# Kernel tuning notes

Hardware: AMD Instinct MI355X
Metric: run time of the kernel (lower is better)

The kernel has to match this reference:

```python
import jax, jax.numpy as jnp
import numpy as np

E, T, D, K = 8, 32768, 1024, 2  # experts, tokens, model dim, topk


def setup_inputs() -> dict:
    key = jax.random.key(0)
    k1, k2, k3, k4 = jax.random.split(key, 4)
    return {
        "tokens": jax.random.normal(k1, (T, D), jnp.float32),
        "router_w": jax.random.normal(k2, (E, D), jnp.float32) * 0.02,
        "w1": jax.random.normal(k3, (E, D, D), jnp.float32) * 0.02,
        "w2": jax.random.normal(k4, (E, D, D), jnp.float32) * 0.02,
    }


def reference(tokens, router_w, w1, w2):
    # Router: softmax over experts, then top-k (order of k irrelevant: combine is a sum)
    scores = jax.nn.softmax(tokens @ router_w.T, axis=-1)          # [T, E]
    topv, topi = jax.lax.top_k(scores, K)                          # [T, K]
    n_tok = tokens.shape[0]
    # Per-token gate weight for each expert (sum of topk weights where index==e).
    gate = jnp.zeros((n_tok, E), tokens.dtype).at[
        jnp.arange(n_tok)[:, None], topi
    ].add(topv)                                                    # [T, E]
    # Dense per-expert MLP, masked/weighted combine == sorted gather + scatter-sum
    out = jnp.zeros_like(tokens)
    for e in range(E):  # fixed small expert count; not a data-dim loop
        h = jax.nn.gelu(tokens @ w1[e], approximate=False)         # [T, D]
        out = out + gate[:, e:e + 1] * (h @ w2[e])                 # [T, D]
    return out
```

## Files before the change

kernel.cpp:

```cpp
#include <hip/hip_runtime.h>
#include <hip/hip_bf16.h>
#include <math.h>
#include <stdint.h>

#define TOK 32768
#define DIM 1024
#define NE 8
#define NSEG 16
#define BMCAP (2 * TOK + NSEG * 256)

#define C_CNT(s) ((s) * 16)
#define C_CUR(s) (256 + (s) * 16)
#define C_SEG(s) (512 + (s))

typedef __attribute__((ext_vector_type(8))) short bf16x8;
typedef __attribute__((ext_vector_type(4))) float f32x4;
typedef unsigned short ushort_t;

__device__ __forceinline__ unsigned short f2b(float x) {
  union { float f; unsigned u; } v; v.f = x;
  unsigned r = v.u + 0x7fffu + ((v.u >> 16) & 1u);
  return (unsigned short)(r >> 16);
}

__device__ __forceinline__ float gelu_fast(float x) {
  const float y2 = -1.5957691216057308f * x * fmaf(0.044715f, x * x, 1.0f);
  return x * __builtin_amdgcn_rcpf(1.0f + __expf(y2));
}

__device__ __forceinline__ void async16(void* lds, const void* g) {
  auto* lp = (__attribute__((address_space(3))) uint32_t*)lds;
  auto* gp = (__attribute__((address_space(1))) uint32_t*)(const_cast<void*>(g));
  __builtin_amdgcn_global_load_lds(gp, lp, 16, 0, 0);
}

__global__ __launch_bounds__(256) void router_seq3(
    const float* __restrict__ tokens, const float* __restrict__ rw,
    int* __restrict__ topi, float* __restrict__ topv) {
  __shared__ float xs[2][32][132];
  __shared__ float wsh[2][8][132];
  __shared__ float sc[256];
  const int tid = threadIdx.x;
  const int e = tid & 7;
  const int tr = tid >> 3;
  const int t0 = blockIdx.x * 32;

  float4 lx0, lx1, lx2, lx3, lw;
  auto issue = [&](int c) {
    const int col = (tid & 31) * 4;
    lx0 = *(const float4*)&tokens[(size_t)(t0 + ((tid + 0) >> 5)) * DIM + c * 128 + col];
    lx1 = *(const float4*)&tokens[(size_t)(t0 + ((tid + 256) >> 5)) * DIM + c * 128 + col];
    lx2 = *(const float4*)&tokens[(size_t)(t0 + ((tid + 512) >> 5)) * DIM + c * 128 + col];
    lx3 = *(const float4*)&tokens[(size_t)(t0 + ((tid + 768) >> 5)) * DIM + c * 128 + col];
    lw  = *(const float4*)&rw[(size_t)(tid >> 5) * DIM + c * 128 + col];
  };
  auto commit = [&](int b) {
    const int col = (tid & 31) * 4;
    *(float4*)&xs[b][(tid + 0) >> 5][col] = lx0;
    *(float4*)&xs[b][(tid + 256) >> 5][col] = lx1;
    *(float4*)&xs[b][(tid + 512) >> 5][col] = lx2;
    *(float4*)&xs[b][(tid + 768) >> 5][col] = lx3;
    *(float4*)&wsh[b][tid >> 5][col] = lw;
  };

  issue(0);
  commit(0);
  __syncthreads();
  float s = 0.f;
  for (int c = 0; c < 8; c++) {
    const int b = c & 1;
    if (c + 1 < 8) issue(c + 1);
#pragma unroll
    for (int k4 = 0; k4 < 32; k4++) {
      const float4 xv = *(const float4*)&xs[b][tr][k4 * 4];
      const float4 wv = *(const float4*)&wsh[b][e][k4 * 4];
      s = fmaf(xv.x, wv.x, s);
      s = fmaf(xv.y, wv.y, s);
      s = fmaf(xv.z, wv.z, s);
      s = fmaf(xv.w, wv.w, s);
    }
    if (c + 1 < 8) commit(b ^ 1);
    __syncthreads();
  }
  sc[tid] = s;
  __syncthreads();
  if (e == 0) {
    float p[NE];
    float m = sc[tr * 8];
#pragma unroll
    for (int i = 1; i < NE; i++) m = fmaxf(m, sc[tr * 8 + i]);
    float sum = 0.f;
#pragma unroll
    for (int i = 0; i < NE; i++) {
      p[i] = expf(sc[tr * 8 + i] - m);
      sum += p[i];
    }
#pragma unroll
    for (int i = 0; i < NE; i++) p[i] = p[i] / sum;
    const int t = t0 + tr;
    int e0 = 0;
#pragma unroll
    for (int i = 1; i < NE; i++) if (p[i] > p[e0]) e0 = i;
    int e1 = (e0 == 0) ? 1 : 0;
#pragma unroll
    for (int i = 0; i < NE; i++) if (i != e0 && p[i] > p[e1]) e1 = i;
    topi[t * 2] = e0;     topv[t * 2] = p[e0];
    topi[t * 2 + 1] = e1; topv[t * 2 + 1] = p[e1];
  }
}

__global__ __launch_bounds__(256) void hist_kernel(const int* __restrict__ topi,
                                                   int* __restrict__ ctrl) {
  __shared__ int h[NSEG];
  const int tid = threadIdx.x;
  if (tid < NSEG) h[tid] = 0;
  __syncthreads();
  const int t = blockIdx.x * 256 + tid;
  atomicAdd(&h[topi[t * 2]], 1);
  atomicAdd(&h[8 + topi[t * 2 + 1]], 1);
  __syncthreads();
  if (tid < NSEG) atomicAdd(&ctrl[C_CNT(tid)], h[tid]);
}

__global__ void prefix_kernel(int* ctrl) {
  if (threadIdx.x == 0 && blockIdx.x == 0) {
    int s = 0;
    for (int g = 0; g < NSEG; g++) {
      ctrl[C_SEG(g)] = s;
      ctrl[C_CUR(g)] = s;
      s += (ctrl[C_CNT(g)] + 255) & ~255;
    }
    ctrl[C_SEG(NSEG)] = s;
  }
}

__global__ __launch_bounds__(256) void init_rows(
    int* __restrict__ row_token, float* __restrict__ row_gate) {
  const int i = blockIdx.x * 256 + threadIdx.x;
  if (i < BMCAP) { row_token[i] = TOK; row_gate[i] = 0.f; }
}

__global__ __launch_bounds__(256) void assign2(
    const int* __restrict__ topi, const float* __restrict__ topv,
    int* __restrict__ ctrl, int* __restrict__ row_token,
    float* __restrict__ row_gate) {
  __shared__ int h[NSEG];
  __shared__ int base[NSEG];
  const int tid = threadIdx.x;
  const int t = blockIdx.x * 256 + tid;
  if (tid < NSEG) h[tid] = 0;
  __syncthreads();
  const int s0 = topi[t * 2], s1 = 8 + topi[t * 2 + 1];
  const int o0 = atomicAdd(&h[s0], 1);
  const int o1 = atomicAdd(&h[s1], 1);
  __syncthreads();
  if (tid < NSEG) base[tid] = atomicAdd(&ctrl[C_CUR(tid)], h[tid]);
  __syncthreads();
  const int p0 = base[s0] + o0, p1 = base[s1] + o1;
  row_token[p0] = t; row_gate[p0] = topv[t * 2];
  row_token[p1] = t; row_gate[p1] = topv[t * 2 + 1];
}

__global__ __launch_bounds__(256) void cast_tokens(
    const float* __restrict__ t, ushort_t* __restrict__ x16) {
  const size_t i = ((size_t)blockIdx.x * 256 + threadIdx.x) * 8;
  const float4 a = *(const float4*)(t + i);
  const float4 b = *(const float4*)(t + i + 4);
  bf16x8 h;
  h[0] = (short)f2b(a.x); h[1] = (short)f2b(a.y);
  h[2] = (short)f2b(a.z); h[3] = (short)f2b(a.w);
  h[4] = (short)f2b(b.x); h[5] = (short)f2b(b.y);
  h[6] = (short)f2b(b.z); h[7] = (short)f2b(b.w);
  *(bf16x8*)(x16 + i) = h;
}

__global__ __launch_bounds__(256) void transpose_cast(
    const float* __restrict__ w, ushort_t* __restrict__ wT) {
  __shared__ float tile[64][65];
  const int e = blockIdx.z;
  const int n0 = blockIdx.x * 64, k0 = blockIdx.y * 64;
  const int tx = threadIdx.x & 63, ty = threadIdx.x >> 6;
  const float* src = w + ((size_t)e << 20);
  ushort_t* dst = wT + ((size_t)e << 20);
#pragma unroll
  for (int r = ty; r < 64; r += 4)
    tile[r][tx] = src[(size_t)(k0 + r) * DIM + n0 + tx];
  __syncthreads();
#pragma unroll
  for (int r = ty; r < 64; r += 4)
    dst[(size_t)(n0 + r) * DIM + k0 + tx] = f2b(tile[tx][r]);
}

template <int PASS, int ADD>
__global__ __launch_bounds__(512, 4) void dgemm(
    const ushort_t* __restrict__ Asrc, const ushort_t* __restrict__ Wt,
    const int* __restrict__ row_token, const float* __restrict__ row_gate,
    const int* __restrict__ ctrl, int s_lo, int s_hi, int chunk,
    ushort_t* __restrict__ Hout, float* __restrict__ out) {
  const int l = (blockIdx.x & 7) * chunk + (blockIdx.x >> 3);
  const int mt = l >> 3, nt = l & 7;
  const int rbase0 = ctrl[C_SEG(s_lo)];
  const int rend = ctrl[C_SEG(s_hi)];
  const int m0 = rbase0 + mt * 256;
  if (m0 >= rend) return;
  const int n0 = nt * 128;
  int sg = s_lo;
  for (int i = s_lo + 1; i < s_hi; i++)
    if (m0 >= ctrl[C_SEG(i)]) sg = i;
  const int e = sg & 7;
  const ushort_t* B = Wt + ((size_t)e << 20);

  __shared__ __align__(16) char smem[49152];
  ushort_t (*As)[8192] = (ushort_t(*)[8192])smem;
  ushort_t (*Bs)[4096] = (ushort_t(*)[4096])(smem + 32768);
  float* scratch = (float*)smem;

  const int tid = threadIdx.x;
  const int lane = tid & 63;
  const int wave = tid >> 6;
  const int wm = wave >> 1, wn = wave & 1;
  const int lr = lane & 15;
  const int kx = (((lane >> 4) ^ (lr & 3) ^ ((lr >> 2) & 3)) << 3);

  const int ko = (((lane & 3) ^ ((lane >> 2) & 3) ^ ((lane >> 4) & 3)) << 3);
  const int ar0 = wave * 32 + (lane >> 2);
  const int brr = wave * 16 + (lane >> 2);
  const ushort_t *asrc0, *asrc1, *bsrc;
  if (PASS == 0) {
    int tk0 = row_token[m0 + ar0];
    int tk1 = row_token[m0 + ar0 + 16];
    if (tk0 >= TOK) tk0 = 0;
    if (tk1 >= TOK) tk1 = 0;
    asrc0 = Asrc + (size_t)tk0 * DIM + ko;
    asrc1 = Asrc + (size_t)tk1 * DIM + ko;
  } else {
    asrc0 = Asrc + (size_t)(m0 + ar0) * DIM + ko;
    asrc1 = Asrc + (size_t)(m0 + ar0 + 16) * DIM + ko;
  }
  bsrc = B + (size_t)(n0 + brr) * DIM + ko;

  f32x4 acc[4][4] = {};

  auto stage = [&](int b, int k0) {
    async16(&As[b][wave * 1024], asrc0 + k0);
    async16(&As[b][wave * 1024 + 512], asrc1 + k0);
    async16(&Bs[b][wave * 512], bsrc + k0);
  };
  auto compute = [&](int b) {
    bf16x8 a[4], bb[4];
#pragma unroll
    for (int mi = 0; mi < 4; mi++)
      a[mi] = *(const bf16x8*)&As[b][(wm * 64 + mi * 16 + lr) * 32 + kx];
#pragma unroll
    for (int ni = 0; ni < 4; ni++)
      bb[ni] = *(const bf16x8*)&Bs[b][(wn * 64 + ni * 16 + lr) * 32 + kx];
#pragma unroll
    for (int mi = 0; mi < 4; mi++)
#pragma unroll
      for (int ni = 0; ni < 4; ni++)
        acc[mi][ni] = __builtin_amdgcn_mfma_f32_16x16x32_bf16(
            a[mi], bb[ni], acc[mi][ni], 0, 0, 0);
  };

  stage(0, 0);
  __syncthreads();
  int cur = 0;
#pragma unroll 1
  for (int t = 0; t < 31; t++) {
    stage(cur ^ 1, (t + 1) * 32);
    compute(cur);
    __syncthreads();
    cur ^= 1;
  }
  compute(cur);
  __syncthreads();

  const int grow = (lane >> 4) << 2;
  const int erow = tid >> 3;
  const int ec0 = (tid & 7) * 16;
#pragma unroll 1
  for (int rnd = 0; rnd < 4; rnd++) {
    if (wm == rnd) {
#pragma unroll
      for (int mi = 0; mi < 4; mi++) {
#pragma unroll
        for (int ni = 0; ni < 4; ni++) {
#pragma unroll
          for (int r = 0; r < 4; r++) {
            const int lrow = mi * 16 + grow + r;
            const int lcol = (wn * 64 + ni * 16 + lr) ^ ((lrow & 3) << 2);
            scratch[lrow * 128 + lcol] = acc[mi][ni][r];
          }
        }
      }
    }
    __syncthreads();
    {
      const int q = (erow & 3) << 2;
      f32x4 v[4];
#pragma unroll
      for (int k = 0; k < 4; k++)
        v[k] = *(const f32x4*)&scratch[erow * 128 + ((ec0 + 4 * k) ^ q)];
      const int rr = m0 + rnd * 64 + erow;
      if (PASS == 0) {
        bf16x8 h0, h1;
#pragma unroll
        for (int k = 0; k < 2; k++)
#pragma unroll
          for (int j = 0; j < 4; j++)
            h0[k * 4 + j] = (short)f2b(gelu_fast(v[k][j]));
#pragma unroll
        for (int k = 0; k < 2; k++)
#pragma unroll
          for (int j = 0; j < 4; j++)
            h1[k * 4 + j] = (short)f2b(gelu_fast(v[2 + k][j]));
        *(bf16x8*)&Hout[(size_t)rr * DIM + n0 + ec0] = h0;
        *(bf16x8*)&Hout[(size_t)rr * DIM + n0 + ec0 + 8] = h1;
      } else {
        const int tok = row_token[rr];
        if (tok < TOK) {
          const float g = row_gate[rr];
          float* op = out + (size_t)tok * DIM + n0 + ec0;
#pragma unroll
          for (int k = 0; k < 4; k++) {
            f32x4 res;
            if (ADD) {
              const f32x4 old = *(const f32x4*)(op + 4 * k);
#pragma unroll
              for (int j = 0; j < 4; j++) res[j] = old[j] + g * v[k][j];
            } else {
#pragma unroll
              for (int j = 0; j < 4; j++) res[j] = g * v[k][j];
            }
            *(f32x4*)(op + 4 * k) = res;
          }
        }
      }
    }
    __syncthreads();
  }
}

extern "C" void kernel_launch(void* const* d_in, const int* in_sizes, int n_in,
                              void* d_out, int out_size, void* d_ws,
                              size_t ws_size, hipStream_t stream) {
  (void)in_sizes; (void)n_in; (void)ws_size; (void)out_size;
  const float* tokens = (const float*)d_in[0];
  const float* rw = (const float*)d_in[1];
  const float* w1 = (const float*)d_in[2];
  const float* w2 = (const float*)d_in[3];
  float* out = (float*)d_out;

  char* ws = (char*)d_ws;
  size_t off = 0;
  auto alloc = [&](size_t b) {
    size_t o = off;
    off += (b + 255) & ~(size_t)255;
    return o;
  };
  int* ctrl = (int*)(ws + alloc(4096));
  int* topi = (int*)(ws + alloc((size_t)TOK * 2 * 4));
  float* topv = (float*)(ws + alloc((size_t)TOK * 2 * 4));
  int* row_token = (int*)(ws + alloc((size_t)BMCAP * 4));
  float* row_gate = (float*)(ws + alloc((size_t)BMCAP * 4));
  ushort_t* X16 = (ushort_t*)(ws + alloc((size_t)TOK * DIM * 2));
  ushort_t* w1T = (ushort_t*)(ws + alloc((size_t)NE * DIM * DIM * 2));
  ushort_t* w2T = (ushort_t*)(ws + alloc((size_t)NE * DIM * DIM * 2));
  ushort_t* H = (ushort_t*)(ws + alloc((size_t)BMCAP * DIM * 2));

  hipMemsetAsync(ctrl, 0, 4096, stream);
  router_seq3<<<TOK / 32, 256, 0, stream>>>(tokens, rw, topi, topv);
  hist_kernel<<<TOK / 256, 256, 0, stream>>>(topi, ctrl);
  prefix_kernel<<<1, 64, 0, stream>>>(ctrl);
  init_rows<<<BMCAP / 256, 256, 0, stream>>>(row_token, row_gate);
  assign2<<<TOK / 256, 256, 0, stream>>>(topi, topv, ctrl, row_token,
                                         row_gate);
  cast_tokens<<<TOK * DIM / 8 / 256, 256, 0, stream>>>(tokens, X16);
  dim3 tg(16, 16, 8);
  transpose_cast<<<tg, 256, 0, stream>>>(w1, w1T);
  transpose_cast<<<tg, 256, 0, stream>>>(w2, w2T);
  dgemm<0, 0><<<2176, 512, 0, stream>>>(X16, w1T, row_token, row_gate, ctrl, 0,
                                        NSEG, 272, H, out);
  dgemm<1, 0><<<1088, 512, 0, stream>>>(H, w2T, row_token, row_gate, ctrl, 0,
                                        8, 136, H, out);
  dgemm<1, 1><<<1088, 512, 0, stream>>>(H, w2T, row_token, row_gate, ctrl, 8,
                                        NSEG, 136, H, out);
}
```

Measured before the change: 608.4 us.

## Write second GEMM to bf16 staging buffer and combine via separate gather kernel

The second expert GEMM no longer scatters gated fp32 results into the output in two ordered launches (store then read-modify-write). It now runs as a single launch over all segments and writes bf16 rows to a staging buffer that aliases the X16/w1T region. A new combine kernel uses an inverse row map to gather each token's two expert rows, weights them, and writes the output once. This removes the fp32 read-modify-write and the serialization between the two halves of the second GEMM. In exchange it adds an extra bf16 round trip and rounds the second GEMM's outputs to bf16 before the gated sum.

```diff
diff --git a/kernel.cpp b/kernel.cpp
--- a/kernel.cpp
+++ b/kernel.cpp
@@ -21,6 +21,12 @@
   union { float f; unsigned u; } v; v.f = x;
   unsigned r = v.u + 0x7fffu + ((v.u >> 16) & 1u);
   return (unsigned short)(r >> 16);
+}
+
+__device__ __forceinline__ float b2f(unsigned short u) {
+  union { unsigned u; float f; } v;
+  v.u = ((unsigned)u) << 16;
+  return v.f;
 }
 
 __device__ __forceinline__ float gelu_fast(float x) {
@@ -134,16 +140,14 @@
   }
 }
 
-__global__ __launch_bounds__(256) void init_rows(
-    int* __restrict__ row_token, float* __restrict__ row_gate) {
+__global__ __launch_bounds__(256) void init_rows(int* __restrict__ row_token) {
   const int i = blockIdx.x * 256 + threadIdx.x;
-  if (i < BMCAP) { row_token[i] = TOK; row_gate[i] = 0.f; }
+  if (i < BMCAP) row_token[i] = TOK;
 }
 
 __global__ __launch_bounds__(256) void assign2(
-    const int* __restrict__ topi, const float* __restrict__ topv,
-    int* __restrict__ ctrl, int* __restrict__ row_token,
-    float* __restrict__ row_gate) {
+    const int* __restrict__ topi, int* __restrict__ ctrl,
+    int* __restrict__ row_token, int* __restrict__ inv) {
   __shared__ int h[NSEG];
   __shared__ int base[NSEG];
   const int tid = threadIdx.x;
@@ -157,8 +161,8 @@
   if (tid < NSEG) base[tid] = atomicAdd(&ctrl[C_CUR(tid)], h[tid]);
   __syncthreads();
   const int p0 = base[s0] + o0, p1 = base[s1] + o1;
-  row_token[p0] = t; row_gate[p0] = topv[t * 2];
-  row_token[p1] = t; row_gate[p1] = topv[t * 2 + 1];
+  row_token[p0] = t; inv[t * 2] = p0;
+  row_token[p1] = t; inv[t * 2 + 1] = p1;
 }
 
 __global__ __launch_bounds__(256) void cast_tokens(
@@ -191,12 +195,34 @@
     dst[(size_t)(n0 + r) * DIM + k0 + tx] = f2b(tile[tx][r]);
 }
 
-template <int PASS, int ADD>
+__global__ __launch_bounds__(256) void combine(
+    const ushort_t* __restrict__ gY, const int* __restrict__ inv,
+    const float* __restrict__ topv, float* __restrict__ out) {
+  const size_t i = (size_t)blockIdx.x * 256 + threadIdx.x;
+  const int t = (int)(i >> 7);
+  const int c = (int)(i & 127) << 3;
+  const int s0 = inv[t * 2], s1 = inv[t * 2 + 1];
+  const float g0 = topv[t * 2], g1 = topv[t * 2 + 1];
+  const bf16x8 y0 = *(const bf16x8*)&gY[(size_t)s0 * DIM + c];
+  const bf16x8 y1 = *(const bf16x8*)&gY[(size_t)s1 * DIM + c];
+  f32x4 o0, o1;
+#pragma unroll
+  for (int j = 0; j < 4; j++)
+    o0[j] = g0 * b2f((unsigned short)y0[j]) + g1 * b2f((unsigned short)y1[j]);
+#pragma unroll
+  for (int j = 0; j < 4; j++)
+    o1[j] = g0 * b2f((unsigned short)y0[4 + j]) +
+            g1 * b2f((unsigned short)y1[4 + j]);
+  float* op = out + (size_t)t * DIM + c;
+  *(f32x4*)op = o0;
+  *(f32x4*)(op + 4) = o1;
+}
+
+template <int PASS>
 __global__ __launch_bounds__(512, 4) void dgemm(
     const ushort_t* __restrict__ Asrc, const ushort_t* __restrict__ Wt,
-    const int* __restrict__ row_token, const float* __restrict__ row_gate,
-    const int* __restrict__ ctrl, int s_lo, int s_hi, int chunk,
-    ushort_t* __restrict__ Hout, float* __restrict__ out) {
+    const int* __restrict__ row_token, const int* __restrict__ ctrl, int s_lo,
+    int s_hi, int chunk, ushort_t* __restrict__ Hout) {
   const int l = (blockIdx.x & 7) * chunk + (blockIdx.x >> 3);
   const int mt = l >> 3, nt = l & 7;
   const int rbase0 = ctrl[C_SEG(s_lo)];
@@ -302,8 +328,8 @@
       for (int k = 0; k < 4; k++)
         v[k] = *(const f32x4*)&scratch[erow * 128 + ((ec0 + 4 * k) ^ q)];
       const int rr = m0 + rnd * 64 + erow;
+      bf16x8 h0, h1;
       if (PASS == 0) {
-        bf16x8 h0, h1;
 #pragma unroll
         for (int k = 0; k < 2; k++)
 #pragma unroll
@@ -314,28 +340,18 @@
 #pragma unroll
           for (int j = 0; j < 4; j++)
             h1[k * 4 + j] = (short)f2b(gelu_fast(v[2 + k][j]));
-        *(bf16x8*)&Hout[(size_t)rr * DIM + n0 + ec0] = h0;
-        *(bf16x8*)&Hout[(size_t)rr * DIM + n0 + ec0 + 8] = h1;
       } else {
-        const int tok = row_token[rr];
-        if (tok < TOK) {
-          const float g = row_gate[rr];
-          float* op = out + (size_t)tok * DIM + n0 + ec0;
-#pragma unroll
-          for (int k = 0; k < 4; k++) {
-            f32x4 res;
-            if (ADD) {
-              const f32x4 old = *(const f32x4*)(op + 4 * k);
-#pragma unroll
-              for (int j = 0; j < 4; j++) res[j] = old[j] + g * v[k][j];
-            } else {
-#pragma unroll
-              for (int j = 0; j < 4; j++) res[j] = g * v[k][j];
-            }
-            *(f32x4*)(op + 4 * k) = res;
-          }
-        }
+#pragma unroll
+        for (int k = 0; k < 2; k++)
+#pragma unroll
+          for (int j = 0; j < 4; j++) h0[k * 4 + j] = (short)f2b(v[k][j]);
+#pragma unroll
+        for (int k = 0; k < 2; k++)
+#pragma unroll
+          for (int j = 0; j < 4; j++) h1[k * 4 + j] = (short)f2b(v[2 + k][j]);
       }
+      *(bf16x8*)&Hout[(size_t)rr * DIM + n0 + ec0] = h0;
+      *(bf16x8*)&Hout[(size_t)rr * DIM + n0 + ec0 + 8] = h1;
     }
     __syncthreads();
   }
@@ -361,28 +377,28 @@
   int* ctrl = (int*)(ws + alloc(4096));
   int* topi = (int*)(ws + alloc((size_t)TOK * 2 * 4));
   float* topv = (float*)(ws + alloc((size_t)TOK * 2 * 4));
+  int* inv = (int*)(ws + alloc((size_t)TOK * 2 * 4));
   int* row_token = (int*)(ws + alloc((size_t)BMCAP * 4));
-  float* row_gate = (float*)(ws + alloc((size_t)BMCAP * 4));
-  ushort_t* X16 = (ushort_t*)(ws + alloc((size_t)TOK * DIM * 2));
-  ushort_t* w1T = (ushort_t*)(ws + alloc((size_t)NE * DIM * DIM * 2));
   ushort_t* w2T = (ushort_t*)(ws + alloc((size_t)NE * DIM * DIM * 2));
   ushort_t* H = (ushort_t*)(ws + alloc((size_t)BMCAP * DIM * 2));
+  const size_t region = alloc((size_t)BMCAP * DIM * 2);
+  ushort_t* X16 = (ushort_t*)(ws + region);
+  ushort_t* w1T = (ushort_t*)(ws + region + (size_t)TOK * DIM * 2);
+  ushort_t* gY = (ushort_t*)(ws + region);
 
   hipMemsetAsync(ctrl, 0, 4096, stream);
   router_seq3<<<TOK / 32, 256, 0, stream>>>(tokens, rw, topi, topv);
   hist_kernel<<<TOK / 256, 256, 0, stream>>>(topi, ctrl);
   prefix_kernel<<<1, 64, 0, stream>>>(ctrl);
-  init_rows<<<BMCAP / 256, 256, 0, stream>>>(row_token, row_gate);
-  assign2<<<TOK / 256, 256, 0, stream>>>(topi, topv, ctrl, row_token,
-                                         row_gate);
+  init_rows<<<BMCAP / 256, 256, 0, stream>>>(row_token);
+  assign2<<<TOK / 256, 256, 0, stream>>>(topi, ctrl, row_token, inv);
   cast_tokens<<<TOK * DIM / 8 / 256, 256, 0, stream>>>(tokens, X16);
   dim3 tg(16, 16, 8);
   transpose_cast<<<tg, 256, 0, stream>>>(w1, w1T);
   transpose_cast<<<tg, 256, 0, stream>>>(w2, w2T);
-  dgemm<0, 0><<<2176, 512, 0, stream>>>(X16, w1T, row_token, row_gate, ctrl, 0,
-                                        NSEG, 272, H, out);
-  dgemm<1, 0><<<1088, 512, 0, stream>>>(H, w2T, row_token, row_gate, ctrl, 0,
-                                        8, 136, H, out);
-  dgemm<1, 1><<<1088, 512, 0, stream>>>(H, w2T, row_token, row_gate, ctrl, 8,
-                                        NSEG, 136, H, out);
-}
+  dgemm<0><<<2176, 512, 0, stream>>>(X16, w1T, row_token, ctrl, 0, NSEG, 272,
+                                     H);
+  dgemm<1><<<2176, 512, 0, stream>>>(H, w2T, row_token, ctrl, 0, NSEG, 272,
+                                     gY);
+  combine<<<TOK * (DIM / 8) / 256, 256, 0, stream>>>(gY, inv, topv, out);
+}
```

Result: faster. 539.4 us (-11.3%).
